# Kernel optimization log

Measured on AMD Instinct MI355X. Metric: run time of the kernel, lower is better.

## Reference

```python
import jax, jax.numpy as jnp
import numpy as np

L = 32       # number of labels (groups)
N = 200000   # number of items (cells)
D = 64       # feature channels


def setup_inputs() -> dict:
    key = jax.random.key(0)
    k_lab, k_x = jax.random.split(key)
    # Each item belongs to exactly one label -> binary membership mask [L, N]
    labels = jax.random.randint(k_lab, (N,), 0, L)
    labmap = (jnp.arange(L)[:, None] == labels[None, :]).astype(jnp.float32)  # [L, N]
    X = jax.random.normal(k_x, (D, N), dtype=jnp.float32)  # [D, N]
    return {"labmap": labmap, "X": X}


def reference(labmap, X):
    # Faithful to LabPool.forward with reduction='max':
    #   prd = labmap.unsqueeze(1) * X  -> [L, D, N]
    #   out = prd.max(2)[0].t()        -> [D, L]
    prd = labmap[:, None, :] * X[None, :, :]  # [L, D, N]
    return jnp.max(prd, axis=2).T  # [D, L]
```

## Files before the change

### kernel.cpp

```cpp
#include <hip/hip_runtime.h>


constexpr int L = 32;
constexpr int D = 64;
constexpr int TI = 64;
constexpr int NB = 1024;
constexpr int XS_STRIDE = 65;
constexpr int SM_STRIDE = 33;
constexpr int SM_SIZE = D * SM_STRIDE;

__global__ __launch_bounds__(256, 4)
void labpool_main(const float* __restrict__ labmap,
                  const float* __restrict__ X,
                  unsigned* __restrict__ tables, int N, int ntiles)
{
    __shared__ float    Xs[D * XS_STRIDE];
    __shared__ unsigned sm[SM_SIZE];

    const int tid  = threadIdx.x;
    const int wave = tid >> 6;
    const int lane = tid & 63;
    const int item  = lane & 15;
    const int lrow0 = (lane >> 4) * 8;

    unsigned* dst = tables + (size_t)blockIdx.x * SM_SIZE;

    if (blockIdx.x >= ntiles) {
        for (int i = tid; i < SM_SIZE; i += 256) dst[i] = 0u;
        return;
    }

    for (int i = tid; i < SM_SIZE; i += 256) sm[i] = 0u;

    const int laneX = lane * XS_STRIDE + wave * 16;
    const int laneS = lane * SM_STRIDE;
    const int d0 = tid >> 4, c4 = 4 * (tid & 15);

    int t = blockIdx.x;

    float4 xr0, xr1, xr2, xr3;
    unsigned labv;
    {
        const float* Xp = X + t * TI;
        xr0 = *reinterpret_cast<const float4*>(Xp + (size_t)(d0)      * N + c4);
        xr1 = *reinterpret_cast<const float4*>(Xp + (size_t)(d0 + 16) * N + c4);
        xr2 = *reinterpret_cast<const float4*>(Xp + (size_t)(d0 + 32) * N + c4);
        xr3 = *reinterpret_cast<const float4*>(Xp + (size_t)(d0 + 48) * N + c4);
        const float* mp = labmap + (size_t)lrow0 * N + t * TI + wave * 16 + item;
        float acc = 0.f;
#pragma unroll
        for (int ll = 0; ll < 8; ++ll)
            acc = fmaf((float)(lrow0 + ll), mp[(size_t)ll * N], acc);
        acc += __shfl_xor(acc, 32);
        acc += __shfl_xor(acc, 16);
        labv = (unsigned)acc;
    }

    while (true) {
        *reinterpret_cast<float4*>(&Xs[(d0)      * XS_STRIDE + c4]) = xr0;
        *reinterpret_cast<float4*>(&Xs[(d0 + 16) * XS_STRIDE + c4]) = xr1;
        *reinterpret_cast<float4*>(&Xs[(d0 + 32) * XS_STRIDE + c4]) = xr2;
        *reinterpret_cast<float4*>(&Xs[(d0 + 48) * XS_STRIDE + c4]) = xr3;
        __syncthreads();

        const int tn = t + NB;
        const bool have_next = (tn < ntiles);

        float acc2 = 0.f;
        if (have_next) {
            const float* Xp = X + tn * TI;
            xr0 = *reinterpret_cast<const float4*>(Xp + (size_t)(d0)      * N + c4);
            xr1 = *reinterpret_cast<const float4*>(Xp + (size_t)(d0 + 16) * N + c4);
            xr2 = *reinterpret_cast<const float4*>(Xp + (size_t)(d0 + 32) * N + c4);
            xr3 = *reinterpret_cast<const float4*>(Xp + (size_t)(d0 + 48) * N + c4);
            const float* mp = labmap + (size_t)lrow0 * N + tn * TI + wave * 16 + item;
#pragma unroll
            for (int ll = 0; ll < 8; ++ll)
                acc2 = fmaf((float)(lrow0 + ll), mp[(size_t)ll * N], acc2);
        }

#pragma unroll
        for (int j = 0; j < 16; ++j) {
            const int labj = __builtin_amdgcn_readlane((int)labv, j);
            const float x = Xs[laneX + j];
            atomicMax(&sm[laneS + labj], __float_as_uint(fmaxf(x, 0.f)));
        }

        if (!have_next) break;

        acc2 += __shfl_xor(acc2, 32);
        acc2 += __shfl_xor(acc2, 16);
        labv = (unsigned)acc2;
        t = tn;
        __syncthreads();
    }

    __syncthreads();
    for (int i = tid; i < SM_SIZE; i += 256) dst[i] = sm[i];
}

__global__ __launch_bounds__(512)
void labpool_reduce(const unsigned* __restrict__ tables, float* __restrict__ out, int nb)
{
    __shared__ unsigned red[16][32];
    const int tid = threadIdx.x;
    const int bq = tid >> 5;
    const int sl = tid & 31;
    const int d  = blockIdx.x;
    unsigned m = 0u;
#pragma unroll 8
    for (int b = bq; b < nb; b += 16) {
        const unsigned v = tables[(size_t)b * SM_SIZE + d * SM_STRIDE + sl];
        m = (v > m) ? v : m;
    }
    red[bq][sl] = m;
    __syncthreads();
    if (bq == 0) {
        unsigned r = red[0][sl];
#pragma unroll
        for (int q = 1; q < 16; ++q) {
            const unsigned v = red[q][sl];
            r = (v > r) ? v : r;
        }
        out[d * L + sl] = __uint_as_float(r);
    }
}

__global__ __launch_bounds__(256)
void labpool_fused_atomic(const float* __restrict__ labmap,
                          const float* __restrict__ X,
                          unsigned* __restrict__ gout, int N)
{
    __shared__ unsigned sm2[D * L];
    __shared__ unsigned char lab[400];
    const int tid = threadIdx.x;
    const int n0 = blockIdx.x * 400;
    for (int i = tid; i < D * L; i += 256) sm2[i] = 0u;
    constexpr int V = 100;
    for (int idx = tid; idx < L * V; idx += 256) {
        const int l = idx / V;
        const int v = idx - l * V;
        const float4 m = *reinterpret_cast<const float4*>(labmap + (size_t)l * N + n0 + 4 * v);
        if (m.x > 0.5f) lab[4 * v + 0] = (unsigned char)l;
        if (m.y > 0.5f) lab[4 * v + 1] = (unsigned char)l;
        if (m.z > 0.5f) lab[4 * v + 2] = (unsigned char)l;
        if (m.w > 0.5f) lab[4 * v + 3] = (unsigned char)l;
    }
    __syncthreads();
    for (int idx = tid; idx < D * V; idx += 256) {
        const int d = idx / V;
        const int v = idx - d * V;
        const float4 x = *reinterpret_cast<const float4*>(X + (size_t)d * N + n0 + 4 * v);
        const uchar4 lv = *reinterpret_cast<const uchar4*>(&lab[4 * v]);
        atomicMax(&sm2[d * L + lv.x], __float_as_uint(fmaxf(x.x, 0.f)));
        atomicMax(&sm2[d * L + lv.y], __float_as_uint(fmaxf(x.y, 0.f)));
        atomicMax(&sm2[d * L + lv.z], __float_as_uint(fmaxf(x.z, 0.f)));
        atomicMax(&sm2[d * L + lv.w], __float_as_uint(fmaxf(x.w, 0.f)));
    }
    __syncthreads();
    for (int i = tid; i < D * L; i += 256) atomicMax(&gout[i], sm2[i]);
}

__global__ void zero_out_k(unsigned* p, int n)
{
    const int i = blockIdx.x * 256 + threadIdx.x;
    if (i < n) p[i] = 0u;
}

extern "C" void kernel_launch(void* const* d_in, const int* in_sizes, int n_in,
                              void* d_out, int out_size, void* d_ws, size_t ws_size,
                              hipStream_t stream)
{
    const float* labmap = (const float*)d_in[0];
    const float* X      = (const float*)d_in[1];
    const int N = in_sizes[0] / L;
    const int ntiles = N / TI;

    const size_t need = (size_t)NB * SM_SIZE * sizeof(unsigned);
    if (d_ws && ws_size >= need && (N % TI) == 0) {
        unsigned* tables = (unsigned*)d_ws;
        labpool_main<<<NB, 256, 0, stream>>>(labmap, X, tables, N, ntiles);
        labpool_reduce<<<D, 512, 0, stream>>>(tables, (float*)d_out, NB);
    } else {
        unsigned* gout = (unsigned*)d_out;
        zero_out_k<<<(D * L + 255) / 256, 256, 0, stream>>>(gout, D * L);
        labpool_fused_atomic<<<N / 400, 256, 0, stream>>>(labmap, X, gout, N);
    }
}
```

Measured before the change: 24.26 us.

## Halve main grid, double threads, double-buffer tile prefetch, vectorize reduce

The main kernel now runs 512 blocks of 512 threads, so each wave handles 8 items per tile instead of 16, and the label decode uses 4 rows per lane with a three-step shuffle reduction. Tile loads become double-buffered two tiles ahead (A/B register sets) to hide global latency behind the shared-memory atomics. Per-block tables are written compactly without padding, and the reduce kernel reads them as uint4 over 128 blocks with a tree reduction. This halves the partial-table traffic and keeps more loads in flight, at the cost of more registers and more barriers per tile.

```diff
diff --git a/kernel.cpp b/kernel.cpp
--- a/kernel.cpp
+++ b/kernel.cpp
@@ -4,12 +4,14 @@
 constexpr int L = 32;
 constexpr int D = 64;
 constexpr int TI = 64;
-constexpr int NB = 1024;
+constexpr int NB = 512;
+constexpr int NT = 512;
 constexpr int XS_STRIDE = 65;
 constexpr int SM_STRIDE = 33;
 constexpr int SM_SIZE = D * SM_STRIDE;
-
-__global__ __launch_bounds__(256, 4)
+constexpr int TBL = D * L;
+
+__global__ __launch_bounds__(NT, 4)
 void labpool_main(const float* __restrict__ labmap,
                   const float* __restrict__ X,
                   unsigned* __restrict__ tables, int N, int ntiles)
@@ -20,109 +22,133 @@
     const int tid  = threadIdx.x;
     const int wave = tid >> 6;
     const int lane = tid & 63;
-    const int item  = lane & 15;
-    const int lrow0 = (lane >> 4) * 8;
-
-    unsigned* dst = tables + (size_t)blockIdx.x * SM_SIZE;
-
-    if (blockIdx.x >= ntiles) {
-        for (int i = tid; i < SM_SIZE; i += 256) dst[i] = 0u;
+    const int item  = lane & 7;
+    const int lrow0 = (lane >> 3) << 2;
+
+    unsigned* dst = tables + (size_t)blockIdx.x * TBL;
+    if ((int)blockIdx.x >= ntiles) {
+        for (int i = tid; i < TBL; i += NT) dst[i] = 0u;
         return;
     }
 
-    for (int i = tid; i < SM_SIZE; i += 256) sm[i] = 0u;
-
-    const int laneX = lane * XS_STRIDE + wave * 16;
+    for (int i = tid; i < SM_SIZE; i += NT) sm[i] = 0u;
+
+    const int r0 = tid >> 4;
+    const int c0 = 4 * (tid & 15);
+    const int r1 = r0 + 32;
+    const size_t rowOff0 = (size_t)r0 * N + c0;
+    const size_t rowOff1 = (size_t)r1 * N + c0;
+    const float* mbase = labmap + (size_t)lrow0 * N + wave * 8 + item;
+
+    const int laneX = lane * XS_STRIDE + wave * 8;
     const int laneS = lane * SM_STRIDE;
-    const int d0 = tid >> 4, c4 = 4 * (tid & 15);
-
-    int t = blockIdx.x;
-
-    float4 xr0, xr1, xr2, xr3;
-    unsigned labv;
-    {
-        const float* Xp = X + t * TI;
-        xr0 = *reinterpret_cast<const float4*>(Xp + (size_t)(d0)      * N + c4);
-        xr1 = *reinterpret_cast<const float4*>(Xp + (size_t)(d0 + 16) * N + c4);
-        xr2 = *reinterpret_cast<const float4*>(Xp + (size_t)(d0 + 32) * N + c4);
-        xr3 = *reinterpret_cast<const float4*>(Xp + (size_t)(d0 + 48) * N + c4);
-        const float* mp = labmap + (size_t)lrow0 * N + t * TI + wave * 16 + item;
-        float acc = 0.f;
+
+    auto LOAD = [&](int t, float4& x0, float4& x1, float (&m)[4]) {
+        const int n0 = t * TI;
+        x0 = *reinterpret_cast<const float4*>(X + rowOff0 + n0);
+        x1 = *reinterpret_cast<const float4*>(X + rowOff1 + n0);
+        const float* mp = mbase + n0;
+        m[0] = mp[0];
+        m[1] = mp[(size_t)N];
+        m[2] = mp[(size_t)2 * N];
+        m[3] = mp[(size_t)3 * N];
+    };
+    auto STAGE = [&](const float4& x0, const float4& x1) {
+        *reinterpret_cast<float4*>(&Xs[r0 * XS_STRIDE + c0]) = x0;
+        *reinterpret_cast<float4*>(&Xs[r1 * XS_STRIDE + c0]) = x1;
+    };
+    auto LABV = [&](const float (&m)[4]) -> unsigned {
+        float acc =            (float)(lrow0)     * m[0];
+        acc = fmaf((float)(lrow0 + 1), m[1], acc);
+        acc = fmaf((float)(lrow0 + 2), m[2], acc);
+        acc = fmaf((float)(lrow0 + 3), m[3], acc);
+        acc += __shfl_xor(acc, 8);
+        acc += __shfl_xor(acc, 16);
+        acc += __shfl_xor(acc, 32);
+        return (unsigned)acc;
+    };
+    auto CONSUME = [&](unsigned labv) {
 #pragma unroll
-        for (int ll = 0; ll < 8; ++ll)
-            acc = fmaf((float)(lrow0 + ll), mp[(size_t)ll * N], acc);
-        acc += __shfl_xor(acc, 32);
-        acc += __shfl_xor(acc, 16);
-        labv = (unsigned)acc;
-    }
-
-    while (true) {
-        *reinterpret_cast<float4*>(&Xs[(d0)      * XS_STRIDE + c4]) = xr0;
-        *reinterpret_cast<float4*>(&Xs[(d0 + 16) * XS_STRIDE + c4]) = xr1;
-        *reinterpret_cast<float4*>(&Xs[(d0 + 32) * XS_STRIDE + c4]) = xr2;
-        *reinterpret_cast<float4*>(&Xs[(d0 + 48) * XS_STRIDE + c4]) = xr3;
-        __syncthreads();
-
-        const int tn = t + NB;
-        const bool have_next = (tn < ntiles);
-
-        float acc2 = 0.f;
-        if (have_next) {
-            const float* Xp = X + tn * TI;
-            xr0 = *reinterpret_cast<const float4*>(Xp + (size_t)(d0)      * N + c4);
-            xr1 = *reinterpret_cast<const float4*>(Xp + (size_t)(d0 + 16) * N + c4);
-            xr2 = *reinterpret_cast<const float4*>(Xp + (size_t)(d0 + 32) * N + c4);
-            xr3 = *reinterpret_cast<const float4*>(Xp + (size_t)(d0 + 48) * N + c4);
-            const float* mp = labmap + (size_t)lrow0 * N + tn * TI + wave * 16 + item;
-#pragma unroll
-            for (int ll = 0; ll < 8; ++ll)
-                acc2 = fmaf((float)(lrow0 + ll), mp[(size_t)ll * N], acc2);
-        }
-
-#pragma unroll
-        for (int j = 0; j < 16; ++j) {
+        for (int j = 0; j < 8; ++j) {
             const int labj = __builtin_amdgcn_readlane((int)labv, j);
             const float x = Xs[laneX + j];
             atomicMax(&sm[laneS + labj], __float_as_uint(fmaxf(x, 0.f)));
         }
-
-        if (!have_next) break;
-
-        acc2 += __shfl_xor(acc2, 32);
-        acc2 += __shfl_xor(acc2, 16);
-        labv = (unsigned)acc2;
-        t = tn;
-        __syncthreads();
-    }
-
-    __syncthreads();
-    for (int i = tid; i < SM_SIZE; i += 256) dst[i] = sm[i];
-}
-
-__global__ __launch_bounds__(512)
+    };
+
+    int t = blockIdx.x;
+    float4 xA0, xA1, xB0, xB1;
+    float mA[4], mB[4];
+    LOAD(t, xA0, xA1, mA);
+    if (t + NB < ntiles) LOAD(t + NB, xB0, xB1, mB);
+
+    while (true) {
+        STAGE(xA0, xA1);
+        const unsigned lvA = LABV(mA);
+        __syncthreads();
+        if (t + 2 * NB < ntiles) LOAD(t + 2 * NB, xA0, xA1, mA);
+        CONSUME(lvA);
+        t += NB;
+        if (t >= ntiles) break;
+        __syncthreads();
+
+        STAGE(xB0, xB1);
+        const unsigned lvB = LABV(mB);
+        __syncthreads();
+        if (t + 2 * NB < ntiles) LOAD(t + 2 * NB, xB0, xB1, mB);
+        CONSUME(lvB);
+        t += NB;
+        if (t >= ntiles) break;
+        __syncthreads();
+    }
+
+    __syncthreads();
+    for (int i = tid; i < TBL; i += NT)
+        dst[i] = sm[(i >> 5) * SM_STRIDE + (i & 31)];
+}
+
+__global__ __launch_bounds__(256)
 void labpool_reduce(const unsigned* __restrict__ tables, float* __restrict__ out, int nb)
 {
-    __shared__ unsigned red[16][32];
-    const int tid = threadIdx.x;
-    const int bq = tid >> 5;
-    const int sl = tid & 31;
-    const int d  = blockIdx.x;
-    unsigned m = 0u;
-#pragma unroll 8
-    for (int b = bq; b < nb; b += 16) {
-        const unsigned v = tables[(size_t)b * SM_SIZE + d * SM_STRIDE + sl];
-        m = (v > m) ? v : m;
-    }
-    red[bq][sl] = m;
-    __syncthreads();
-    if (bq == 0) {
-        unsigned r = red[0][sl];
+    __shared__ uint4 red[256];
+    const int tid  = threadIdx.x;
+    const int d    = blockIdx.x >> 1;
+    const int h    = blockIdx.x & 1;
+    const int part = tid & 3;
+    const int g    = tid >> 2;
+    const int base = d * L + h * 16 + part * 4;
+
+    uint4 m = make_uint4(0u, 0u, 0u, 0u);
+    for (int b = g; b < nb; b += 64) {
+        const uint4 v = *reinterpret_cast<const uint4*>(tables + (size_t)b * TBL + base);
+        m.x = (v.x > m.x) ? v.x : m.x;
+        m.y = (v.y > m.y) ? v.y : m.y;
+        m.z = (v.z > m.z) ? v.z : m.z;
+        m.w = (v.w > m.w) ? v.w : m.w;
+    }
+    red[tid] = m;
+    __syncthreads();
 #pragma unroll
-        for (int q = 1; q < 16; ++q) {
-            const unsigned v = red[q][sl];
-            r = (v > r) ? v : r;
+    for (int s = 128; s >= 4; s >>= 1) {
+        if (tid < s) {
+            const uint4 v = red[tid + s];
+            uint4 r = red[tid];
+            r.x = (v.x > r.x) ? v.x : r.x;
+            r.y = (v.y > r.y) ? v.y : r.y;
+            r.z = (v.z > r.z) ? v.z : r.z;
+            r.w = (v.w > r.w) ? v.w : r.w;
+            red[tid] = r;
         }
-        out[d * L + sl] = __uint_as_float(r);
+        __syncthreads();
+    }
+    if (tid < 4) {
+        const uint4 r = red[tid];
+        float4 f;
+        f.x = __uint_as_float(r.x);
+        f.y = __uint_as_float(r.y);
+        f.z = __uint_as_float(r.z);
+        f.w = __uint_as_float(r.w);
+        *reinterpret_cast<float4*>(out + d * L + h * 16 + tid * 4) = f;
     }
 }
 
@@ -176,11 +202,11 @@
     const int N = in_sizes[0] / L;
     const int ntiles = N / TI;
 
-    const size_t need = (size_t)NB * SM_SIZE * sizeof(unsigned);
+    const size_t need = (size_t)NB * TBL * sizeof(unsigned);
     if (d_ws && ws_size >= need && (N % TI) == 0) {
         unsigned* tables = (unsigned*)d_ws;
-        labpool_main<<<NB, 256, 0, stream>>>(labmap, X, tables, N, ntiles);
-        labpool_reduce<<<D, 512, 0, stream>>>(tables, (float*)d_out, NB);
+        labpool_main<<<NB, NT, 0, stream>>>(labmap, X, tables, N, ntiles);
+        labpool_reduce<<<2 * D, 256, 0, stream>>>(tables, (float*)d_out, NB);
     } else {
         unsigned* gout = (unsigned*)d_out;
         zero_out_k<<<(D * L + 255) / 256, 256, 0, stream>>>(gout, D * L);
```

Result: faster. 22.35 us (-7.9%).
